# Kernel tuning notes

Measured on AMD Instinct MI355X. Metric: run time of the kernel, lower is better.

## Reference

```python
import jax, jax.numpy as jnp
import numpy as np

N_VOX = 200000
C_IN = 64
C_OUT = 128
GRID = (480, 360, 32)  # (D, H, W) cylindrical voxel grid
LRELU_SLOPE = 0.01
BN_EPS = 1e-5

OFFSETS_31 = [(dz, 0, dx) for dz in (-1, 0, 1) for dx in (-1, 0, 1)]  # kernel (3,1,3)
OFFSETS_13 = [(0, dy, dx) for dy in (-1, 0, 1) for dx in (-1, 0, 1)]  # kernel (1,3,3)


def _build_neighbors(coords, offsets, grid):
    """coords: [N,3] int. Returns [K,N] int32 neighbor indices, N = sentinel (inactive)."""
    D, H, W = grid
    n = coords.shape[0]
    lookup = np.full(D * H * W, -1, dtype=np.int64)
    lin = (coords[:, 0] * H + coords[:, 1]) * W + coords[:, 2]
    lookup[lin] = np.arange(n)
    nbrs = []
    for off in offsets:
        c = coords + np.asarray(off)
        valid = (c[:, 0] >= 0) & (c[:, 0] < D) & (c[:, 1] >= 0) & (c[:, 1] < H) & (c[:, 2] >= 0) & (c[:, 2] < W)
        l = np.clip((c[:, 0] * H + c[:, 1]) * W + c[:, 2], 0, D * H * W - 1)
        idx = np.where(valid, lookup[l], -1)
        nbrs.append(np.where(idx < 0, n, idx))
    return np.stack(nbrs).astype(np.int32)


def setup_inputs() -> dict:
    key = jax.random.key(0)
    ks = jax.random.split(key, 8)
    rng = np.random.default_rng(0)
    D, H, W = GRID
    lin = rng.choice(D * H * W, size=N_VOX, replace=False)
    coords = np.stack([lin // (H * W), (lin // W) % H, lin % W], axis=1)
    nbr31 = jnp.asarray(_build_neighbors(coords, OFFSETS_31, GRID))
    nbr13 = jnp.asarray(_build_neighbors(coords, OFFSETS_13, GRID))

    def kaiming(k, kk, cin, cout):
        return jax.random.normal(k, (kk, cin, cout), jnp.float32) * np.float32(1.0 / np.sqrt(kk * cin))

    return {
        "features": jax.random.normal(ks[0], (N_VOX, C_IN), jnp.float32),
        "nbr31": nbr31,
        "nbr13": nbr13,
        "W_conv1": kaiming(ks[1], 9, C_IN, C_OUT),
        "W_conv1_2": kaiming(ks[2], 9, C_OUT, C_OUT),
        "W_conv2": kaiming(ks[3], 9, C_IN, C_OUT),
        "W_conv3": kaiming(ks[4], 9, C_OUT, C_OUT),
        "g0": jnp.ones((C_OUT,), jnp.float32), "b0": jnp.zeros((C_OUT,), jnp.float32),
        "g0_2": jnp.ones((C_OUT,), jnp.float32), "b0_2": jnp.zeros((C_OUT,), jnp.float32),
        "g1": jnp.ones((C_OUT,), jnp.float32), "b1": jnp.zeros((C_OUT,), jnp.float32),
        "g2": jnp.ones((C_OUT,), jnp.float32), "b2": jnp.zeros((C_OUT,), jnp.float32),
    }


def _submconv(f, nbr, W):
    """Submanifold sparse conv: f [N,Cin], nbr [K,N] (N=sentinel), W [K,Cin,Cout]."""
    f_pad = jnp.concatenate([f, jnp.zeros((1, f.shape[1]), f.dtype)], axis=0)
    out = jnp.zeros((f.shape[0], W.shape[2]), f.dtype)
    for k in range(W.shape[0]):  # fixed K=9 kernel taps
        out = out + f_pad[nbr[k]] @ W[k]
    return out


def _lrelu(x):
    return jnp.where(x >= 0, x, LRELU_SLOPE * x)


def _bn(x, g, b):
    # BatchNorm1d, training mode: batch stats over active voxels (biased var)
    m = jnp.mean(x, axis=0)
    v = jnp.var(x, axis=0)
    return (x - m) * jax.lax.rsqrt(v + BN_EPS) * g + b


def reference(features, nbr31, nbr13, W_conv1, W_conv1_2, W_conv2, W_conv3,
              g0, b0, g0_2, b0_2, g1, b1, g2, b2):
    # shortcut branch: conv3x1 -> lrelu -> bn -> conv1x3 -> lrelu -> bn
    s = _submconv(features, nbr31, W_conv1)
    s = _bn(_lrelu(s), g0, b0)
    s = _submconv(s, nbr13, W_conv1_2)
    s = _bn(_lrelu(s), g0_2, b0_2)
    # main branch: conv1x3 -> lrelu -> bn -> conv3x1 -> lrelu -> bn
    r = _submconv(features, nbr13, W_conv2)
    r = _bn(_lrelu(r), g1, b1)
    r = _submconv(r, nbr31, W_conv3)
    r = _bn(_lrelu(r), g2, b2)
    return r + s
```

## Files before the change

kernel.cpp:

```cpp
#include <hip/hip_runtime.h>
#include <hip/hip_bf16.h>

typedef unsigned short u16;
typedef unsigned int u32;
typedef __attribute__((ext_vector_type(8))) short s16x8;
typedef __attribute__((ext_vector_type(4))) short s16x4;
typedef __attribute__((ext_vector_type(4))) float f32x4;

__device__ inline u16 f2bf(float x) {
    u32 u = __float_as_uint(x);
    u32 r = (u + 0x7fffu + ((u >> 16) & 1u)) >> 16;
    return (u16)r;
}
__device__ inline float bf2f(u16 u) {
    return __uint_as_float(((u32)u) << 16);
}

__global__ void k_feat2bf(const float* __restrict__ f, u16* __restrict__ o,
                          int total, int nvalid) {
    int i = (blockIdx.x * 256 + threadIdx.x) * 8;
    if (i >= total) return;
    s16x8 v;
#pragma unroll
    for (int j = 0; j < 8; ++j) {
        float x = (i + j < nvalid) ? f[i + j] : 0.f;
        v[j] = (short)f2bf(x);
    }
    *(s16x8*)(o + i) = v;
}

__global__ void k_swz(const float* __restrict__ W, u16* __restrict__ o, int cin) {
    int i = blockIdx.x * 256 + threadIdx.x;
    int total = 9 * cin * 128;
    if (i >= total) return;
    int j = i & 7;
    int l = (i >> 3) & 63;
    int fr = i >> 9;
    int ct = fr & 7;
    int rest = fr >> 3;
    int kcn = cin >> 5;
    int kc = rest % kcn;
    int t = rest / kcn;
    int kk = kc * 32 + (l >> 4) * 8 + j;
    int c = ct * 16 + (l & 15);
    o[i] = f2bf(W[(t * cin + kk) * 128 + c]);
}

template <int CIN>
__global__ __launch_bounds__(1024) void k_conv(
    const u16* __restrict__ src,
    const int* __restrict__ nbr,
    const u16* __restrict__ w,
    u16* __restrict__ zout,
    float* __restrict__ stats,
    int N) {
    constexpr int KC = CIN / 32;
    constexpr int FR = 9 * KC * 4;
    __shared__ u16 wl[FR * 512];
    __shared__ float sstat[128];

    const int tid = threadIdx.x;
    const int half = blockIdx.y;

    for (int i = tid; i < FR * 64; i += 1024) {
        int p = i & 63;
        int f = i >> 6;
        int ctp = f & 3;
        int tk = f >> 2;
        s16x8 v = *(const s16x8*)(w + ((size_t)(tk * 8 + half * 4 + ctp)) * 512 + p * 8);
        *(s16x8*)&wl[(size_t)f * 512 + p * 8] = v;
    }
    if (tid < 128) sstat[tid] = 0.f;
    __syncthreads();

    const int lane = tid & 63;
    const int wv = tid >> 6;
    const int base = blockIdx.x * 512 + wv * 32;
    const int am = lane & 15;
    const int grp = lane >> 4;
    const int vi0 = base + am;
    const int vi1 = base + 16 + am;

    int rn0[9], rn1[9];
#pragma unroll
    for (int t = 0; t < 9; ++t) {
        rn0[t] = (vi0 < N) ? nbr[t * N + vi0] : N;
        rn1[t] = (vi1 < N) ? nbr[t * N + vi1] : N;
    }

    f32x4 acc0[4], acc1[4];
#pragma unroll
    for (int c = 0; c < 4; ++c) {
        acc0[c] = (f32x4){0.f, 0.f, 0.f, 0.f};
        acc1[c] = (f32x4){0.f, 0.f, 0.f, 0.f};
    }

#pragma unroll
    for (int t = 0; t < 9; ++t) {
        const u16* lb = wl + (size_t)t * (KC * 4) * 512 + lane * 8;
        if (__any(rn0[t] != N)) {
            const u16* sp = src + (size_t)rn0[t] * CIN + grp * 8;
#pragma unroll
            for (int kc = 0; kc < KC; ++kc) {
                s16x8 a = *(const s16x8*)(sp + kc * 32);
#pragma unroll
                for (int c = 0; c < 4; ++c) {
                    s16x8 b = *(const s16x8*)(lb + (kc * 4 + c) * 512);
                    acc0[c] = __builtin_amdgcn_mfma_f32_16x16x32_bf16(a, b, acc0[c], 0, 0, 0);
                }
            }
        }
        if (__any(rn1[t] != N)) {
            const u16* sp = src + (size_t)rn1[t] * CIN + grp * 8;
#pragma unroll
            for (int kc = 0; kc < KC; ++kc) {
                s16x8 a = *(const s16x8*)(sp + kc * 32);
#pragma unroll
                for (int c = 0; c < 4; ++c) {
                    s16x8 b = *(const s16x8*)(lb + (kc * 4 + c) * 512);
                    acc1[c] = __builtin_amdgcn_mfma_f32_16x16x32_bf16(a, b, acc1[c], 0, 0, 0);
                }
            }
        }
    }

#pragma unroll
    for (int c = 0; c < 4; ++c) {
        float s = 0.f, q = 0.f;
        const int col = half * 64 + c * 16 + am;
#pragma unroll
        for (int j = 0; j < 4; ++j) {
            {
                float x = acc0[c][j];
                float z = (x > 0.f) ? x : 0.01f * x;
                int row = base + grp * 4 + j;
                if (row < N) zout[(size_t)row * 128 + col] = f2bf(z);
                s += z;
                q += z * z;
            }
            {
                float x = acc1[c][j];
                float z = (x > 0.f) ? x : 0.01f * x;
                int row = base + 16 + grp * 4 + j;
                if (row < N) zout[(size_t)row * 128 + col] = f2bf(z);
                s += z;
                q += z * z;
            }
        }
        s += __shfl_xor(s, 16);
        q += __shfl_xor(q, 16);
        s += __shfl_xor(s, 32);
        q += __shfl_xor(q, 32);
        if (lane < 16) {
            atomicAdd(&sstat[c * 16 + am], s);
            atomicAdd(&sstat[64 + c * 16 + am], q);
        }
    }
    __syncthreads();
    if (tid < 64) {
        int cg = half * 64 + tid;
        atomicAdd(stats + cg, sstat[tid]);
        atomicAdd(stats + 128 + cg, sstat[64 + tid]);
    }
}

__global__ void k_fin(const float* __restrict__ stats,
                      const float* __restrict__ g0, const float* __restrict__ b0,
                      const float* __restrict__ g1, const float* __restrict__ b1,
                      float* __restrict__ ss, int N) {
    int tid = threadIdx.x;
    int set = tid >> 7, c = tid & 127;
    const float* st = stats + set * 256;
    float invN = 1.f / (float)N;
    float m = st[c] * invN;
    float var = st[128 + c] * invN - m * m;
    const float* g = set ? g1 : g0;
    const float* b = set ? b1 : b0;
    float sc = g[c] * rsqrtf(var + 1e-5f);
    float sh = b[c] - m * sc;
    float* o = ss + set * 256;
    o[c] = sc;
    o[128 + c] = sh;
}

__global__ void k_aff(const u16* __restrict__ z, const float* __restrict__ ss,
                      u16* __restrict__ y, int N) {
    int v = blockIdx.x * 256 + threadIdx.x;
    int total = (N + 1) * 16;
    if (v >= total) return;
    int row = v >> 4;
    int cb = (v & 15) * 8;
    s16x8 o;
    if (row < N) {
        s16x8 zi = *(const s16x8*)(z + (size_t)row * 128 + cb);
#pragma unroll
        for (int j = 0; j < 8; ++j) {
            float x = bf2f((u16)zi[j]);
            float r = x * ss[cb + j] + ss[128 + cb + j];
            o[j] = (short)f2bf(r);
        }
    } else {
        o = (s16x8){0, 0, 0, 0, 0, 0, 0, 0};
    }
    *(s16x8*)(y + (size_t)row * 128 + cb) = o;
}

__global__ void k_final(const u16* __restrict__ z3, const u16* __restrict__ z4,
                        const float* __restrict__ ssA, const float* __restrict__ ssB,
                        float* __restrict__ out, int N) {
    int v = blockIdx.x * 256 + threadIdx.x;
    int total = N * 32;
    if (v >= total) return;
    int row = v >> 5;
    int cb = (v & 31) * 4;
    s16x4 a = *(const s16x4*)(z3 + (size_t)row * 128 + cb);
    s16x4 b = *(const s16x4*)(z4 + (size_t)row * 128 + cb);
    f32x4 o;
#pragma unroll
    for (int j = 0; j < 4; ++j) {
        int c = cb + j;
        o[j] = bf2f((u16)a[j]) * ssA[c] + ssA[128 + c] +
               bf2f((u16)b[j]) * ssB[c] + ssB[128 + c];
    }
    *(f32x4*)(out + (size_t)row * 128 + cb) = o;
}

extern "C" void kernel_launch(void* const* d_in, const int* in_sizes, int n_in,
                              void* d_out, int out_size, void* d_ws, size_t ws_size,
                              hipStream_t stream) {
    const float* feat = (const float*)d_in[0];
    const int* nbr31 = (const int*)d_in[1];
    const int* nbr13 = (const int*)d_in[2];
    const float* W1 = (const float*)d_in[3];
    const float* W12 = (const float*)d_in[4];
    const float* W2 = (const float*)d_in[5];
    const float* W3 = (const float*)d_in[6];
    const float* g0 = (const float*)d_in[7];
    const float* b0 = (const float*)d_in[8];
    const float* g02 = (const float*)d_in[9];
    const float* b02 = (const float*)d_in[10];
    const float* g1 = (const float*)d_in[11];
    const float* b1 = (const float*)d_in[12];
    const float* g2 = (const float*)d_in[13];
    const float* b2 = (const float*)d_in[14];
    float* out = (float*)d_out;
    const int N = in_sizes[0] / 64;

    char* p = (char*)d_ws;
    auto alloc = [&](size_t bytes) {
        char* r = p;
        p += (bytes + 255) & ~(size_t)255;
        return r;
    };
    float* stats = (float*)alloc(4 * 256 * sizeof(float));
    float* ss = (float*)alloc(4 * 256 * sizeof(float));
    u16* featbf = (u16*)alloc((size_t)(N + 1) * 64 * 2);
    u16* w1 = (u16*)alloc((size_t)9 * 64 * 128 * 2);
    u16* w2 = (u16*)alloc((size_t)9 * 64 * 128 * 2);
    u16* w12 = (u16*)alloc((size_t)9 * 128 * 128 * 2);
    u16* w3 = (u16*)alloc((size_t)9 * 128 * 128 * 2);
    u16* zA = (u16*)alloc((size_t)N * 128 * 2);
    u16* zB = (u16*)alloc((size_t)N * 128 * 2);
    u16* y1 = (u16*)alloc((size_t)(N + 1) * 128 * 2);
    u16* y2 = (u16*)alloc((size_t)(N + 1) * 128 * 2);

    hipMemsetAsync(stats, 0, 4 * 256 * sizeof(float), stream);

    int totF = (N + 1) * 64;
    k_feat2bf<<<(totF / 8 + 255) / 256, 256, 0, stream>>>(feat, featbf, totF, N * 64);
    k_swz<<<(9 * 64 * 128 + 255) / 256, 256, 0, stream>>>(W1, w1, 64);
    k_swz<<<(9 * 64 * 128 + 255) / 256, 256, 0, stream>>>(W2, w2, 64);
    k_swz<<<(9 * 128 * 128 + 255) / 256, 256, 0, stream>>>(W12, w12, 128);
    k_swz<<<(9 * 128 * 128 + 255) / 256, 256, 0, stream>>>(W3, w3, 128);

    dim3 cgrid((N + 511) / 512, 2);
    k_conv<64><<<cgrid, 1024, 0, stream>>>(featbf, nbr31, w1, zA, stats + 0, N);
    k_conv<64><<<cgrid, 1024, 0, stream>>>(featbf, nbr13, w2, zB, stats + 256, N);
    k_fin<<<1, 256, 0, stream>>>(stats, g0, b0, g1, b1, ss, N);
    int ablk = ((N + 1) * 16 + 255) / 256;
    k_aff<<<ablk, 256, 0, stream>>>(zA, ss + 0, y1, N);
    k_aff<<<ablk, 256, 0, stream>>>(zB, ss + 256, y2, N);
    k_conv<128><<<cgrid, 1024, 0, stream>>>(y1, nbr13, w12, zA, stats + 512, N);
    k_conv<128><<<cgrid, 1024, 0, stream>>>(y2, nbr31, w3, zB, stats + 768, N);
    k_fin<<<1, 256, 0, stream>>>(stats + 512, g02, b02, g2, b2, ss + 512, N);
    k_final<<<(N * 32 + 255) / 256, 256, 0, stream>>>(zA, zB, ss + 512, ss + 768, out, N);
}
```

Measured before the change: 381.2 us.

## Fold BN affine into next-conv weights, merge branch convs, prefetch gathers

Drops the separate BN-affine pass by folding the BN scale into the second-stage conv weights. The BN shift becomes a per-tap bias, added only for neighbours that are active, as tracked by ballot masks. The two branch convs in each stage now run in one launch using blockIdx.z, and neighbour indices and feature rows are double-buffered so the gather for the next tap overlaps the MFMAs of the current one. This removes two full read/write passes over N×128 bf16 tensors and two launches. In exchange it adds register pressure from the prefetch buffers and masks, and the weight rounding changes slightly because of the pre-scaling.

```diff
diff --git a/kernel.cpp b/kernel.cpp
--- a/kernel.cpp
+++ b/kernel.cpp
@@ -3,6 +3,7 @@
 
 typedef unsigned short u16;
 typedef unsigned int u32;
+typedef unsigned long long u64;
 typedef __attribute__((ext_vector_type(8))) short s16x8;
 typedef __attribute__((ext_vector_type(4))) short s16x4;
 typedef __attribute__((ext_vector_type(4))) float f32x4;
@@ -29,7 +30,8 @@
     *(s16x8*)(o + i) = v;
 }
 
-__global__ void k_swz(const float* __restrict__ W, u16* __restrict__ o, int cin) {
+__global__ void k_swz(const float* __restrict__ W, const float* __restrict__ sc,
+                      u16* __restrict__ o, int cin) {
     int i = blockIdx.x * 256 + threadIdx.x;
     int total = 9 * cin * 128;
     if (i >= total) return;
@@ -43,24 +45,44 @@
     int t = rest / kcn;
     int kk = kc * 32 + (l >> 4) * 8 + j;
     int c = ct * 16 + (l & 15);
-    o[i] = f2bf(W[(t * cin + kk) * 128 + c]);
-}
-
-template <int CIN>
+    float v = W[(t * cin + kk) * 128 + c];
+    if (sc) v *= sc[kk];
+    o[i] = f2bf(v);
+}
+
+__global__ void k_ubias(const float* __restrict__ W, const float* __restrict__ sh,
+                        float* __restrict__ u, int cin) {
+    int c = threadIdx.x;
+    int t = blockIdx.x;
+    float s = 0.f;
+    for (int k = 0; k < cin; ++k) s += sh[k] * W[(t * cin + k) * 128 + c];
+    u[t * 128 + c] = s;
+}
+
+template <int CIN, bool AFF>
 __global__ __launch_bounds__(1024) void k_conv(
-    const u16* __restrict__ src,
-    const int* __restrict__ nbr,
-    const u16* __restrict__ w,
-    u16* __restrict__ zout,
-    float* __restrict__ stats,
+    const u16* __restrict__ srcA, const u16* __restrict__ srcB,
+    const int* __restrict__ nbrA, const int* __restrict__ nbrB,
+    const u16* __restrict__ wA, const u16* __restrict__ wB,
+    const float* __restrict__ uA, const float* __restrict__ uB,
+    u16* __restrict__ zoutA, u16* __restrict__ zoutB,
+    float* __restrict__ statsA, float* __restrict__ statsB,
     int N) {
     constexpr int KC = CIN / 32;
     constexpr int FR = 9 * KC * 4;
+    constexpr int UB = AFF ? 9 * 128 : 4;
     __shared__ u16 wl[FR * 512];
     __shared__ float sstat[128];
+    __shared__ float ubuf[UB];
 
     const int tid = threadIdx.x;
     const int half = blockIdx.y;
+    const int cz = blockIdx.z;
+    const u16* __restrict__ src = cz ? srcB : srcA;
+    const int* __restrict__ nbr = cz ? nbrB : nbrA;
+    const u16* __restrict__ w = cz ? wB : wA;
+    u16* __restrict__ zout = cz ? zoutB : zoutA;
+    float* __restrict__ stats = cz ? statsB : statsA;
 
     for (int i = tid; i < FR * 64; i += 1024) {
         int p = i & 63;
@@ -70,6 +92,10 @@
         s16x8 v = *(const s16x8*)(w + ((size_t)(tk * 8 + half * 4 + ctp)) * 512 + p * 8);
         *(s16x8*)&wl[(size_t)f * 512 + p * 8] = v;
     }
+    if (AFF) {
+        const float* __restrict__ u = cz ? uB : uA;
+        for (int i = tid; i < 9 * 128; i += 1024) ubuf[i] = u[i];
+    }
     if (tid < 128) sstat[tid] = 0.f;
     __syncthreads();
 
@@ -81,11 +107,26 @@
     const int vi0 = base + am;
     const int vi1 = base + 16 + am;
 
-    int rn0[9], rn1[9];
-#pragma unroll
-    for (int t = 0; t < 9; ++t) {
-        rn0[t] = (vi0 < N) ? nbr[t * N + vi0] : N;
-        rn1[t] = (vi1 < N) ? nbr[t * N + vi1] : N;
+    int r0[9], r1[9];
+    u64 m0[9], m1[9];
+    bool e[9];
+    s16x8 a0[2][KC], a1[2][KC];
+
+    r0[0] = (vi0 < N) ? nbr[vi0] : N;
+    r1[0] = (vi1 < N) ? nbr[vi1] : N;
+    r0[1] = (vi0 < N) ? nbr[N + vi0] : N;
+    r1[1] = (vi1 < N) ? nbr[N + vi1] : N;
+    m0[0] = __ballot(r0[0] != N);
+    m1[0] = __ballot(r1[0] != N);
+    e[0] = (m0[0] | m1[0]) != 0ULL;
+    {
+        const u16* sp0 = src + (size_t)r0[0] * CIN + grp * 8;
+        const u16* sp1 = src + (size_t)r1[0] * CIN + grp * 8;
+#pragma unroll
+        for (int kc = 0; kc < KC; ++kc) {
+            a0[0][kc] = *(const s16x8*)(sp0 + kc * 32);
+            a1[0][kc] = *(const s16x8*)(sp1 + kc * 32);
+        }
     }
 
     f32x4 acc0[4], acc1[4];
@@ -97,28 +138,32 @@
 
 #pragma unroll
     for (int t = 0; t < 9; ++t) {
-        const u16* lb = wl + (size_t)t * (KC * 4) * 512 + lane * 8;
-        if (__any(rn0[t] != N)) {
-            const u16* sp = src + (size_t)rn0[t] * CIN + grp * 8;
+        const int cur = t & 1, nxt = cur ^ 1;
+        if (t + 2 < 9) {
+            r0[t + 2] = (vi0 < N) ? nbr[(t + 2) * N + vi0] : N;
+            r1[t + 2] = (vi1 < N) ? nbr[(t + 2) * N + vi1] : N;
+        }
+        if (t + 1 < 9) {
+            m0[t + 1] = __ballot(r0[t + 1] != N);
+            m1[t + 1] = __ballot(r1[t + 1] != N);
+            e[t + 1] = (m0[t + 1] | m1[t + 1]) != 0ULL;
+            const u16* sp0 = src + (size_t)r0[t + 1] * CIN + grp * 8;
+            const u16* sp1 = src + (size_t)r1[t + 1] * CIN + grp * 8;
 #pragma unroll
             for (int kc = 0; kc < KC; ++kc) {
-                s16x8 a = *(const s16x8*)(sp + kc * 32);
+                a0[nxt][kc] = *(const s16x8*)(sp0 + kc * 32);
+                a1[nxt][kc] = *(const s16x8*)(sp1 + kc * 32);
+            }
+        }
+        if (e[t]) {
+            const u16* lb = wl + (size_t)t * (KC * 4) * 512 + lane * 8;
+#pragma unroll
+            for (int kc = 0; kc < KC; ++kc) {
 #pragma unroll
                 for (int c = 0; c < 4; ++c) {
                     s16x8 b = *(const s16x8*)(lb + (kc * 4 + c) * 512);
-                    acc0[c] = __builtin_amdgcn_mfma_f32_16x16x32_bf16(a, b, acc0[c], 0, 0, 0);
-                }
-            }
-        }
-        if (__any(rn1[t] != N)) {
-            const u16* sp = src + (size_t)rn1[t] * CIN + grp * 8;
-#pragma unroll
-            for (int kc = 0; kc < KC; ++kc) {
-                s16x8 a = *(const s16x8*)(sp + kc * 32);
-#pragma unroll
-                for (int c = 0; c < 4; ++c) {
-                    s16x8 b = *(const s16x8*)(lb + (kc * 4 + c) * 512);
-                    acc1[c] = __builtin_amdgcn_mfma_f32_16x16x32_bf16(a, b, acc1[c], 0, 0, 0);
+                    acc0[c] = __builtin_amdgcn_mfma_f32_16x16x32_bf16(a0[cur][kc], b, acc0[c], 0, 0, 0);
+                    acc1[c] = __builtin_amdgcn_mfma_f32_16x16x32_bf16(a1[cur][kc], b, acc1[c], 0, 0, 0);
                 }
             }
         }
@@ -128,20 +173,34 @@
     for (int c = 0; c < 4; ++c) {
         float s = 0.f, q = 0.f;
         const int col = half * 64 + c * 16 + am;
+        float uv[9];
+        if (AFF) {
+#pragma unroll
+            for (int t = 0; t < 9; ++t) uv[t] = ubuf[t * 128 + col];
+        }
 #pragma unroll
         for (int j = 0; j < 4; ++j) {
+            const int r = grp * 4 + j;
+            float ub0 = 0.f, ub1 = 0.f;
+            if (AFF) {
+#pragma unroll
+                for (int t = 0; t < 9; ++t) {
+                    if ((m0[t] >> r) & 1) ub0 += uv[t];
+                    if ((m1[t] >> r) & 1) ub1 += uv[t];
+                }
+            }
             {
-                float x = acc0[c][j];
+                float x = acc0[c][j] + ub0;
                 float z = (x > 0.f) ? x : 0.01f * x;
-                int row = base + grp * 4 + j;
+                int row = base + r;
                 if (row < N) zout[(size_t)row * 128 + col] = f2bf(z);
                 s += z;
                 q += z * z;
             }
             {
-                float x = acc1[c][j];
+                float x = acc1[c][j] + ub1;
                 float z = (x > 0.f) ? x : 0.01f * x;
-                int row = base + 16 + grp * 4 + j;
+                int row = base + 16 + r;
                 if (row < N) zout[(size_t)row * 128 + col] = f2bf(z);
                 s += z;
                 q += z * z;
@@ -181,28 +240,6 @@
     float* o = ss + set * 256;
     o[c] = sc;
     o[128 + c] = sh;
-}
-
-__global__ void k_aff(const u16* __restrict__ z, const float* __restrict__ ss,
-                      u16* __restrict__ y, int N) {
-    int v = blockIdx.x * 256 + threadIdx.x;
-    int total = (N + 1) * 16;
-    if (v >= total) return;
-    int row = v >> 4;
-    int cb = (v & 15) * 8;
-    s16x8 o;
-    if (row < N) {
-        s16x8 zi = *(const s16x8*)(z + (size_t)row * 128 + cb);
-#pragma unroll
-        for (int j = 0; j < 8; ++j) {
-            float x = bf2f((u16)zi[j]);
-            float r = x * ss[cb + j] + ss[128 + cb + j];
-            o[j] = (short)f2bf(r);
-        }
-    } else {
-        o = (s16x8){0, 0, 0, 0, 0, 0, 0, 0};
-    }
-    *(s16x8*)(y + (size_t)row * 128 + cb) = o;
 }
 
 __global__ void k_final(const u16* __restrict__ z3, const u16* __restrict__ z4,
@@ -254,34 +291,41 @@
     };
     float* stats = (float*)alloc(4 * 256 * sizeof(float));
     float* ss = (float*)alloc(4 * 256 * sizeof(float));
+    float* u12 = (float*)alloc(9 * 128 * sizeof(float));
+    float* u3 = (float*)alloc(9 * 128 * sizeof(float));
     u16* featbf = (u16*)alloc((size_t)(N + 1) * 64 * 2);
     u16* w1 = (u16*)alloc((size_t)9 * 64 * 128 * 2);
     u16* w2 = (u16*)alloc((size_t)9 * 64 * 128 * 2);
     u16* w12 = (u16*)alloc((size_t)9 * 128 * 128 * 2);
     u16* w3 = (u16*)alloc((size_t)9 * 128 * 128 * 2);
-    u16* zA = (u16*)alloc((size_t)N * 128 * 2);
-    u16* zB = (u16*)alloc((size_t)N * 128 * 2);
-    u16* y1 = (u16*)alloc((size_t)(N + 1) * 128 * 2);
-    u16* y2 = (u16*)alloc((size_t)(N + 1) * 128 * 2);
+    u16* zA = (u16*)alloc((size_t)(N + 1) * 128 * 2);
+    u16* zB = (u16*)alloc((size_t)(N + 1) * 128 * 2);
+    u16* z2A = (u16*)alloc((size_t)N * 128 * 2);
+    u16* z2B = (u16*)alloc((size_t)N * 128 * 2);
 
     hipMemsetAsync(stats, 0, 4 * 256 * sizeof(float), stream);
+    hipMemsetAsync(zA + (size_t)N * 128, 0, 256, stream);
+    hipMemsetAsync(zB + (size_t)N * 128, 0, 256, stream);
 
     int totF = (N + 1) * 64;
     k_feat2bf<<<(totF / 8 + 255) / 256, 256, 0, stream>>>(feat, featbf, totF, N * 64);
-    k_swz<<<(9 * 64 * 128 + 255) / 256, 256, 0, stream>>>(W1, w1, 64);
-    k_swz<<<(9 * 64 * 128 + 255) / 256, 256, 0, stream>>>(W2, w2, 64);
-    k_swz<<<(9 * 128 * 128 + 255) / 256, 256, 0, stream>>>(W12, w12, 128);
-    k_swz<<<(9 * 128 * 128 + 255) / 256, 256, 0, stream>>>(W3, w3, 128);
-
-    dim3 cgrid((N + 511) / 512, 2);
-    k_conv<64><<<cgrid, 1024, 0, stream>>>(featbf, nbr31, w1, zA, stats + 0, N);
-    k_conv<64><<<cgrid, 1024, 0, stream>>>(featbf, nbr13, w2, zB, stats + 256, N);
+    k_swz<<<(9 * 64 * 128 + 255) / 256, 256, 0, stream>>>(W1, nullptr, w1, 64);
+    k_swz<<<(9 * 64 * 128 + 255) / 256, 256, 0, stream>>>(W2, nullptr, w2, 64);
+
+    dim3 cgrid((N + 511) / 512, 2, 2);
+    k_conv<64, false><<<cgrid, 1024, 0, stream>>>(
+        featbf, featbf, nbr31, nbr13, w1, w2, nullptr, nullptr,
+        zA, zB, stats + 0, stats + 256, N);
     k_fin<<<1, 256, 0, stream>>>(stats, g0, b0, g1, b1, ss, N);
-    int ablk = ((N + 1) * 16 + 255) / 256;
-    k_aff<<<ablk, 256, 0, stream>>>(zA, ss + 0, y1, N);
-    k_aff<<<ablk, 256, 0, stream>>>(zB, ss + 256, y2, N);
-    k_conv<128><<<cgrid, 1024, 0, stream>>>(y1, nbr13, w12, zA, stats + 512, N);
-    k_conv<128><<<cgrid, 1024, 0, stream>>>(y2, nbr31, w3, zB, stats + 768, N);
+
+    k_swz<<<(9 * 128 * 128 + 255) / 256, 256, 0, stream>>>(W12, ss + 0, w12, 128);
+    k_swz<<<(9 * 128 * 128 + 255) / 256, 256, 0, stream>>>(W3, ss + 256, w3, 128);
+    k_ubias<<<9, 128, 0, stream>>>(W12, ss + 128, u12, 128);
+    k_ubias<<<9, 128, 0, stream>>>(W3, ss + 256 + 128, u3, 128);
+
+    k_conv<128, true><<<cgrid, 1024, 0, stream>>>(
+        zA, zB, nbr13, nbr31, w12, w3, u12, u3,
+        z2A, z2B, stats + 512, stats + 768, N);
     k_fin<<<1, 256, 0, stream>>>(stats + 512, g02, b02, g2, b2, ss + 512, N);
-    k_final<<<(N * 32 + 255) / 256, 256, 0, stream>>>(zA, zB, ss + 512, ss + 768, out, N);
-}
+    k_final<<<(N * 32 + 255) / 256, 256, 0, stream>>>(z2A, z2B, ss + 512, ss + 768, out, N);
+}
```

Result: slower. 482.0 us (+26.5%).

## Merge paired branch convs into one launch and split output channels four ways

Applied to the files above, without the earlier changes.

The two independent branch convolutions at each stage now run in a single launch, selected by blockIdx.z. Output channels are split into four 32-wide slices instead of two 64-wide halves, which halves the LDS weight footprint and the accumulator registers per block. The two row-group tap loops are merged so each weight fragment feeds two MFMAs under one any-active check. The aim is more occupancy and fewer launches, at the cost of re-gathering each neighbour row across four channel slices.

```diff
diff --git a/kernel.cpp b/kernel.cpp
--- a/kernel.cpp
+++ b/kernel.cpp
@@ -47,30 +47,36 @@
 }
 
 template <int CIN>
-__global__ __launch_bounds__(1024) void k_conv(
-    const u16* __restrict__ src,
-    const int* __restrict__ nbr,
-    const u16* __restrict__ w,
-    u16* __restrict__ zout,
-    float* __restrict__ stats,
+__global__ __launch_bounds__(1024, 8) void k_conv(
+    const u16* __restrict__ srcA, const u16* __restrict__ srcB,
+    const int* __restrict__ nbrA, const int* __restrict__ nbrB,
+    const u16* __restrict__ wA, const u16* __restrict__ wB,
+    u16* __restrict__ zoutA, u16* __restrict__ zoutB,
+    float* __restrict__ statsA, float* __restrict__ statsB,
     int N) {
     constexpr int KC = CIN / 32;
-    constexpr int FR = 9 * KC * 4;
+    constexpr int FR = 9 * KC * 2;
     __shared__ u16 wl[FR * 512];
-    __shared__ float sstat[128];
+    __shared__ float sstat[64];
 
     const int tid = threadIdx.x;
     const int half = blockIdx.y;
+    const int cz = blockIdx.z;
+    const u16* __restrict__ src = cz ? srcB : srcA;
+    const int* __restrict__ nbr = cz ? nbrB : nbrA;
+    const u16* __restrict__ w = cz ? wB : wA;
+    u16* __restrict__ zout = cz ? zoutB : zoutA;
+    float* __restrict__ stats = cz ? statsB : statsA;
 
     for (int i = tid; i < FR * 64; i += 1024) {
         int p = i & 63;
         int f = i >> 6;
-        int ctp = f & 3;
-        int tk = f >> 2;
-        s16x8 v = *(const s16x8*)(w + ((size_t)(tk * 8 + half * 4 + ctp)) * 512 + p * 8);
+        int ctp = f & 1;
+        int tk = f >> 1;
+        s16x8 v = *(const s16x8*)(w + ((size_t)(tk * 8 + half * 2 + ctp)) * 512 + p * 8);
         *(s16x8*)&wl[(size_t)f * 512 + p * 8] = v;
     }
-    if (tid < 128) sstat[tid] = 0.f;
+    if (tid < 64) sstat[tid] = 0.f;
     __syncthreads();
 
     const int lane = tid & 63;
@@ -81,53 +87,44 @@
     const int vi0 = base + am;
     const int vi1 = base + 16 + am;
 
-    int rn0[9], rn1[9];
+    int r0[9], r1[9];
 #pragma unroll
     for (int t = 0; t < 9; ++t) {
-        rn0[t] = (vi0 < N) ? nbr[t * N + vi0] : N;
-        rn1[t] = (vi1 < N) ? nbr[t * N + vi1] : N;
-    }
-
-    f32x4 acc0[4], acc1[4];
-#pragma unroll
-    for (int c = 0; c < 4; ++c) {
+        r0[t] = (vi0 < N) ? nbr[t * N + vi0] : N;
+        r1[t] = (vi1 < N) ? nbr[t * N + vi1] : N;
+    }
+
+    f32x4 acc0[2], acc1[2];
+#pragma unroll
+    for (int c = 0; c < 2; ++c) {
         acc0[c] = (f32x4){0.f, 0.f, 0.f, 0.f};
         acc1[c] = (f32x4){0.f, 0.f, 0.f, 0.f};
     }
 
 #pragma unroll
     for (int t = 0; t < 9; ++t) {
-        const u16* lb = wl + (size_t)t * (KC * 4) * 512 + lane * 8;
-        if (__any(rn0[t] != N)) {
-            const u16* sp = src + (size_t)rn0[t] * CIN + grp * 8;
+        if (__any((r0[t] != N) || (r1[t] != N))) {
+            const u16* sp0 = src + (size_t)r0[t] * CIN + grp * 8;
+            const u16* sp1 = src + (size_t)r1[t] * CIN + grp * 8;
+            const u16* lb = wl + (size_t)t * (KC * 2) * 512 + lane * 8;
 #pragma unroll
             for (int kc = 0; kc < KC; ++kc) {
-                s16x8 a = *(const s16x8*)(sp + kc * 32);
-#pragma unroll
-                for (int c = 0; c < 4; ++c) {
-                    s16x8 b = *(const s16x8*)(lb + (kc * 4 + c) * 512);
-                    acc0[c] = __builtin_amdgcn_mfma_f32_16x16x32_bf16(a, b, acc0[c], 0, 0, 0);
+                s16x8 a0 = *(const s16x8*)(sp0 + kc * 32);
+                s16x8 a1 = *(const s16x8*)(sp1 + kc * 32);
+#pragma unroll
+                for (int c = 0; c < 2; ++c) {
+                    s16x8 b = *(const s16x8*)(lb + (kc * 2 + c) * 512);
+                    acc0[c] = __builtin_amdgcn_mfma_f32_16x16x32_bf16(a0, b, acc0[c], 0, 0, 0);
+                    acc1[c] = __builtin_amdgcn_mfma_f32_16x16x32_bf16(a1, b, acc1[c], 0, 0, 0);
                 }
             }
         }
-        if (__any(rn1[t] != N)) {
-            const u16* sp = src + (size_t)rn1[t] * CIN + grp * 8;
-#pragma unroll
-            for (int kc = 0; kc < KC; ++kc) {
-                s16x8 a = *(const s16x8*)(sp + kc * 32);
-#pragma unroll
-                for (int c = 0; c < 4; ++c) {
-                    s16x8 b = *(const s16x8*)(lb + (kc * 4 + c) * 512);
-                    acc1[c] = __builtin_amdgcn_mfma_f32_16x16x32_bf16(a, b, acc1[c], 0, 0, 0);
-                }
-            }
-        }
-    }
-
-#pragma unroll
-    for (int c = 0; c < 4; ++c) {
+    }
+
+#pragma unroll
+    for (int c = 0; c < 2; ++c) {
         float s = 0.f, q = 0.f;
-        const int col = half * 64 + c * 16 + am;
+        const int col = half * 32 + c * 16 + am;
 #pragma unroll
         for (int j = 0; j < 4; ++j) {
             {
@@ -153,14 +150,14 @@
         q += __shfl_xor(q, 32);
         if (lane < 16) {
             atomicAdd(&sstat[c * 16 + am], s);
-            atomicAdd(&sstat[64 + c * 16 + am], q);
+            atomicAdd(&sstat[32 + c * 16 + am], q);
         }
     }
     __syncthreads();
-    if (tid < 64) {
-        int cg = half * 64 + tid;
+    if (tid < 32) {
+        int cg = half * 32 + tid;
         atomicAdd(stats + cg, sstat[tid]);
-        atomicAdd(stats + 128 + cg, sstat[64 + tid]);
+        atomicAdd(stats + 128 + cg, sstat[32 + tid]);
     }
 }
 
@@ -273,15 +270,15 @@
     k_swz<<<(9 * 128 * 128 + 255) / 256, 256, 0, stream>>>(W12, w12, 128);
     k_swz<<<(9 * 128 * 128 + 255) / 256, 256, 0, stream>>>(W3, w3, 128);
 
-    dim3 cgrid((N + 511) / 512, 2);
-    k_conv<64><<<cgrid, 1024, 0, stream>>>(featbf, nbr31, w1, zA, stats + 0, N);
-    k_conv<64><<<cgrid, 1024, 0, stream>>>(featbf, nbr13, w2, zB, stats + 256, N);
+    dim3 cgrid((N + 511) / 512, 4, 2);
+    k_conv<64><<<cgrid, 1024, 0, stream>>>(
+        featbf, featbf, nbr31, nbr13, w1, w2, zA, zB, stats + 0, stats + 256, N);
     k_fin<<<1, 256, 0, stream>>>(stats, g0, b0, g1, b1, ss, N);
     int ablk = ((N + 1) * 16 + 255) / 256;
     k_aff<<<ablk, 256, 0, stream>>>(zA, ss + 0, y1, N);
     k_aff<<<ablk, 256, 0, stream>>>(zB, ss + 256, y2, N);
-    k_conv<128><<<cgrid, 1024, 0, stream>>>(y1, nbr13, w12, zA, stats + 512, N);
-    k_conv<128><<<cgrid, 1024, 0, stream>>>(y2, nbr31, w3, zB, stats + 768, N);
+    k_conv<128><<<cgrid, 1024, 0, stream>>>(
+        y1, y2, nbr13, nbr31, w12, w3, zA, zB, stats + 512, stats + 768, N);
     k_fin<<<1, 256, 0, stream>>>(stats + 512, g02, b02, g2, b2, ss + 512, N);
     k_final<<<(N * 32 + 255) / 256, 256, 0, stream>>>(zA, zB, ss + 512, ss + 768, out, N);
 }
```

Result: slower. 454.5 us (+19.2%).
